# Optimization experiments

Hardware: AMD Instinct MI355X
Metric: run time of the kernel (lower is better)

The kernel has to match this reference:

```python
import jax, jax.numpy as jnp
import numpy as np

B, L, WD = 4096, 30, 300          # batch of news, title length, word dim
H, AD = 20, 20                    # attention heads, per-head dim
MD = H * AD                       # multi_dim = 400
E, ED = 10, 100                   # entities per news, entity dim
QD = 200                          # query_vector_dim
CAT, CD = 18, 50                  # category vocab / dim
SUB, SD = 300, 50                 # subcategory vocab / dim


def _mha(x, wq, bq, wk, bk, wv, bv):
    # x: [B, L, Din] -> [B, L, MD]; standard multi-head self-attention
    b, l, _ = x.shape
    q = (x @ wq + bq).reshape(b, l, H, AD)
    k = (x @ wk + bk).reshape(b, l, H, AD)
    v = (x @ wv + bv).reshape(b, l, H, AD)
    scores = jnp.einsum('blhd,bmhd->bhlm', q, k) / jnp.sqrt(jnp.asarray(AD, x.dtype))
    attn = jax.nn.softmax(scores, axis=-1)
    out = jnp.einsum('bhlm,bmhd->blhd', attn, v)
    return out.reshape(b, l, MD)


def _layernorm(x, g, b):
    mu = jnp.mean(x, axis=-1, keepdims=True)
    var = jnp.var(x, axis=-1, keepdims=True)
    return (x - mu) / jnp.sqrt(var + 1e-5) * g + b


def _additive(x, w, b, q):
    # x: [B, L, D] -> [B, D]
    scores = jnp.tanh(x @ w + b) @ q            # [B, L]
    alpha = jax.nn.softmax(scores, axis=-1)
    return jnp.einsum('bl,bld->bd', alpha, x)


def setup_inputs() -> dict:
    key = jax.random.key(0)
    ks = iter(jax.random.split(key, 40))
    n = lambda shape, s=0.02: (jax.random.normal(next(ks), shape, dtype=jnp.float32) * s)
    inp = {
        'word_embedding': jax.random.normal(next(ks), (B, L, WD), dtype=jnp.float32),
        'entity_embedding': jax.random.normal(next(ks), (B, E, ED), dtype=jnp.float32),
        'category_index': jax.random.randint(next(ks), (B,), 0, CAT, dtype=jnp.int64 if jax.config.jax_enable_x64 else jnp.int32),
        'subcategory_index': jax.random.randint(next(ks), (B,), 0, SUB, dtype=jnp.int64 if jax.config.jax_enable_x64 else jnp.int32),
        # category / subcategory branches
        'emb_cat': n((CAT, CD), 1.0), 'fc1_w': n((CD, MD)), 'fc1_b': jnp.zeros((MD,), jnp.float32),
        'emb_sub': n((SUB, SD), 1.0), 'fc2_w': n((SD, MD)), 'fc2_b': jnp.zeros((MD,), jnp.float32),
        # word multi-head self-attention
        'wq': n((WD, MD)), 'bq': jnp.zeros((MD,), jnp.float32),
        'wk': n((WD, MD)), 'bk': jnp.zeros((MD,), jnp.float32),
        'wv': n((WD, MD)), 'bv': jnp.zeros((MD,), jnp.float32),
        # shared LayerNorm
        'ln_g': jnp.ones((MD,), jnp.float32), 'ln_b': jnp.zeros((MD,), jnp.float32),
        # word additive attention
        'wa_w': n((MD, QD)), 'wa_b': jnp.zeros((QD,), jnp.float32), 'wa_q': n((QD,), 1.0),
        # entity branch: fc3 + GCN (learnable adjacency over the E entities of a news)
        'fc3_w': n((ED, ED)), 'fc3_b': jnp.zeros((ED,), jnp.float32),
        'gcn_A': n((E, E), 1.0), 'gcn_w': n((ED, MD)), 'gcn_b': jnp.zeros((MD,), jnp.float32),
        'ea_w': n((MD, QD)), 'ea_b': jnp.zeros((QD,), jnp.float32), 'ea_q': n((QD,), 1.0),
        # final news-level additive attention over 4 views
        'na_w': n((MD, QD)), 'na_b': jnp.zeros((QD,), jnp.float32), 'na_q': n((QD,), 1.0),
    }
    return inp


def reference(word_embedding, entity_embedding, category_index, subcategory_index,
              emb_cat, fc1_w, fc1_b, emb_sub, fc2_w, fc2_b,
              wq, bq, wk, bk, wv, bv, ln_g, ln_b,
              wa_w, wa_b, wa_q, fc3_w, fc3_b, gcn_A, gcn_w, gcn_b,
              ea_w, ea_b, ea_q, na_w, na_b, na_q):
    # category / subcategory reps (dropout is identity in eval)
    cat_rep = jnp.tanh(emb_cat[category_index] @ fc1_w + fc1_b)      # [B, MD]
    sub_rep = jnp.tanh(emb_sub[subcategory_index] @ fc2_w + fc2_b)   # [B, MD]
    # word branch
    w = _mha(word_embedding, wq, bq, wk, bk, wv, bv)                 # [B, L, MD]
    w = _layernorm(w, ln_g, ln_b)
    word_rep = jnp.tanh(_additive(w, wa_w, wa_b, wa_q))              # [B, MD]
    # entity branch: fc3 -> intra-news GCN -> shared LayerNorm
    e = jnp.tanh(entity_embedding @ fc3_w + fc3_b)                   # [B, E, ED]
    e = jax.nn.relu(jnp.einsum('ef,bfd->bed', gcn_A, e) @ gcn_w + gcn_b)  # [B, E, MD]
    e = _layernorm(e, ln_g, ln_b)
    ent_rep = jnp.tanh(_additive(e, ea_w, ea_b, ea_q))               # [B, MD]
    # fuse the 4 views with additive attention
    views = jnp.stack([word_rep, ent_rep, cat_rep, sub_rep], axis=1)  # [B, 4, MD]
    news_rep = jnp.tanh(_additive(views, na_w, na_b, na_q))          # [B, MD]
    return news_rep
```

## Files before the change

### kernel.cpp

```cpp
#include <hip/hip_runtime.h>
#include <hip/hip_bf16.h>
#include <math.h>

#define B_  4096
#define L_  30
#define WD_ 300
#define H_  20
#define AD_ 20
#define MD_ 400
#define E_  10
#define ED_ 100
#define QD_ 200
#define CD_ 50
#define SD_ 50

typedef unsigned short ushort_t;
typedef __attribute__((ext_vector_type(8))) short bf16x8_t;
typedef __attribute__((ext_vector_type(4))) float f32x4_t;

#define SX_STR   328
#define QKV_STR  1218
#define OUTB_STR 424
#define SOUT_STR 401
#define P_STR    40
#define WT_K     320
#define WAT_K    416

#define N_WT    (1200 * WT_K)
#define N_WAT   (208 * WAT_K)
#define N_FC3T  (112 * 128)
#define N_GCNT  (400 * 128)
#define N_EAT   (208 * WAT_K)

union FragU {
  unsigned  u[4];
  short     s[8];
  bf16x8_t  h;
};

__device__ __forceinline__ ushort_t f2bf(float f) {
  unsigned u = __builtin_bit_cast(unsigned, f);
  unsigned r = (u + 0x7fffu + ((u >> 16) & 1u)) >> 16;
  return (ushort_t)r;
}
__device__ __forceinline__ float bf2f(ushort_t h) {
  return __builtin_bit_cast(float, ((unsigned)h) << 16);
}
__device__ __forceinline__ float wave_reduce_sum(float v) {
  #pragma unroll
  for (int off = 32; off > 0; off >>= 1) v += __shfl_xor(v, off);
  return v;
}
__device__ __forceinline__ void split2(float v, ushort_t* __restrict__ H,
                                       ushort_t* __restrict__ Lo, int idx) {
  const ushort_t h = f2bf(v);
  H[idx] = h;
  Lo[idx] = f2bf(v - bf2f(h));
}

__global__ __launch_bounds__(256) void prep_weights(
    const float* __restrict__ wq, const float* __restrict__ wk, const float* __restrict__ wv,
    const float* __restrict__ wa_w, const float* __restrict__ fc3_w,
    const float* __restrict__ gcn_w, const float* __restrict__ ea_w,
    ushort_t* __restrict__ Wt, ushort_t* __restrict__ Wat,
    ushort_t* __restrict__ fc3TH, ushort_t* __restrict__ fc3TL,
    ushort_t* __restrict__ gcnTH, ushort_t* __restrict__ gcnTL,
    ushort_t* __restrict__ eaTH, ushort_t* __restrict__ eaTL)
{
  int idx = blockIdx.x * 256 + threadIdx.x;
  if (idx < N_WT) {
    const int n = idx / WT_K, k = idx - n * WT_K;
    float v = 0.f;
    if (k < WD_) {
      const float* w = (n < 400) ? wq : (n < 800) ? wk : wv;
      const int c = (n < 400) ? n : (n < 800) ? n - 400 : n - 800;
      v = w[k * MD_ + c];
    }
    Wt[idx] = f2bf(v);
    return;
  }
  idx -= N_WT;
  if (idx < N_WAT) {
    const int q = idx / WAT_K, d = idx - q * WAT_K;
    Wat[idx] = (q < QD_ && d < MD_) ? f2bf(wa_w[d * QD_ + q]) : (ushort_t)0;
    return;
  }
  idx -= N_WAT;
  if (idx < N_FC3T) {
    const int n = idx / 128, k = idx - n * 128;
    const float v = (n < ED_ && k < ED_) ? fc3_w[k * ED_ + n] : 0.f;
    split2(v, fc3TH, fc3TL, idx);
    return;
  }
  idx -= N_FC3T;
  if (idx < N_GCNT) {
    const int n = idx / 128, k = idx - n * 128;
    const float v = (k < ED_) ? gcn_w[k * MD_ + n] : 0.f;
    split2(v, gcnTH, gcnTL, idx);
    return;
  }
  idx -= N_GCNT;
  if (idx < N_EAT) {
    const int q = idx / WAT_K, d = idx - q * WAT_K;
    const float v = (q < QD_ && d < MD_) ? ea_w[d * QD_ + q] : 0.f;
    split2(v, eaTH, eaTL, idx);
  }
}

__global__ __launch_bounds__(1024, 4) void word_branch_kernel(
    const float* __restrict__ X,
    const ushort_t* __restrict__ Wt, const ushort_t* __restrict__ Wat,
    const float* __restrict__ bq, const float* __restrict__ bk, const float* __restrict__ bv,
    const float* __restrict__ ln_g, const float* __restrict__ ln_b,
    const float* __restrict__ wa_b, const float* __restrict__ wa_q,
    float* __restrict__ word_rep)
{
  __shared__ __align__(16) union {
    ushort_t x[32 * SX_STR];
    ushort_t p[16 * 16 * P_STR];
  } uA;
  __shared__ __align__(16) union {
    ushort_t qkv[30 * QKV_STR];
    ushort_t o[32 * OUTB_STR];
  } uB;
  __shared__ __align__(16) float sOut[30 * SOUT_STR];
  __shared__ float sSc[32];
  __shared__ float sAlpha[32];

  const int b    = blockIdx.x;
  const int tid  = threadIdx.x;
  const int wave = tid >> 6;
  const int lane = tid & 63;
  const int lr   = lane & 15;
  const int kg   = lane >> 4;

  const float* xb = X + (size_t)b * (L_ * WD_);
  {
    const int r = tid >> 5;
    const int c0 = tid & 31;
    #pragma unroll
    for (int k = 0; k < 10; ++k) {
      const int c = c0 + k * 32;
      const float v = (r < L_ && c < WD_) ? xb[r * WD_ + c] : 0.f;
      uA.x[r * SX_STR + c] = f2bf(v);
    }
  }
  if (tid < 32) sSc[tid] = 0.f;
  __syncthreads();

  for (int nt = wave; nt < 75; nt += 16) {
    const ushort_t* wbase = &Wt[(nt * 16 + lr) * WT_K + kg * 8];
    bf16x8_t bfa[10];
    #pragma unroll
    for (int ks = 0; ks < 10; ++ks)
      bfa[ks] = *reinterpret_cast<const bf16x8_t*>(wbase + ks * 32);
    f32x4_t acc0 = {0,0,0,0}, acc1 = {0,0,0,0};
    #pragma unroll
    for (int ks = 0; ks < 10; ++ks) {
      const int kb = ks * 32 + kg * 8;
      bf16x8_t af0 = *reinterpret_cast<const bf16x8_t*>(&uA.x[lr * SX_STR + kb]);
      bf16x8_t af1 = *reinterpret_cast<const bf16x8_t*>(&uA.x[(16 + lr) * SX_STR + kb]);
      acc0 = __builtin_amdgcn_mfma_f32_16x16x32_bf16(af0, bfa[ks], acc0, 0, 0, 0);
      acc1 = __builtin_amdgcn_mfma_f32_16x16x32_bf16(af1, bfa[ks], acc1, 0, 0, 0);
    }
    const int col = nt * 16 + lr;
    const float bias = (col < 400) ? bq[col] : (col < 800) ? bk[col - 400] : bv[col - 800];
    #pragma unroll
    for (int i = 0; i < 4; ++i) {
      uB.qkv[(kg * 4 + i) * QKV_STR + col] = f2bf(acc0[i] + bias);
      const int r2 = 16 + kg * 4 + i;
      if (r2 < L_) uB.qkv[r2 * QKV_STR + col] = f2bf(acc1[i] + bias);
    }
  }
  __syncthreads();

  ushort_t* pw = &uA.p[wave * (16 * P_STR)];
  for (int u = wave; u < 2 * H_; u += 16) {
    const int h = u >> 1, mt = u & 1;
    const int hq = h * AD_, hk = 400 + h * AD_, hv = 800 + h * AD_;

    bf16x8_t aq, bkf[2];
    {
      FragU fq;
      fq.u[0]=fq.u[1]=fq.u[2]=fq.u[3]=0;
      const bool okrow = (mt == 0) || (lr < 14);
      if (okrow && kg < 3) {
        const ushort_t* pq = &uB.qkv[(mt * 16 + lr) * QKV_STR + hq + kg * 8];
        fq.u[0] = *(const unsigned*)(pq);     fq.u[1] = *(const unsigned*)(pq + 2);
        if (kg < 2) { fq.u[2] = *(const unsigned*)(pq + 4); fq.u[3] = *(const unsigned*)(pq + 6); }
      }
      aq = fq.h;
    }
    #pragma unroll
    for (int t = 0; t < 2; ++t) {
      FragU fk;
      fk.u[0]=fk.u[1]=fk.u[2]=fk.u[3]=0;
      const bool okrow = (t == 0) || (lr < 14);
      if (okrow && kg < 3) {
        const ushort_t* pk = &uB.qkv[(t * 16 + lr) * QKV_STR + hk + kg * 8];
        fk.u[0] = *(const unsigned*)(pk);     fk.u[1] = *(const unsigned*)(pk + 2);
        if (kg < 2) { fk.u[2] = *(const unsigned*)(pk + 4); fk.u[3] = *(const unsigned*)(pk + 6); }
      }
      bkf[t] = fk.h;
    }
    f32x4_t c0 = {0,0,0,0}, c1 = {0,0,0,0};
    c0 = __builtin_amdgcn_mfma_f32_16x16x32_bf16(aq, bkf[0], c0, 0, 0, 0);
    c1 = __builtin_amdgcn_mfma_f32_16x16x32_bf16(aq, bkf[1], c1, 0, 0, 0);

    const float SCALE = 0.2236067977499790f;
    #pragma unroll
    for (int i = 0; i < 4; ++i) {
      const float v0 = c0[i] * SCALE;
      const float v1 = (lr < 14) ? c1[i] * SCALE : -1e30f;
      float mx = fmaxf(v0, v1);
      mx = fmaxf(mx, __shfl_xor(mx, 1));
      mx = fmaxf(mx, __shfl_xor(mx, 2));
      mx = fmaxf(mx, __shfl_xor(mx, 4));
      mx = fmaxf(mx, __shfl_xor(mx, 8));
      const float e0 = __expf(v0 - mx);
      const float e1 = (lr < 14) ? __expf(v1 - mx) : 0.f;
      float s = e0 + e1;
      s += __shfl_xor(s, 1);
      s += __shfl_xor(s, 2);
      s += __shfl_xor(s, 4);
      s += __shfl_xor(s, 8);
      const float inv = 1.f / s;
      const int row = kg * 4 + i;
      pw[row * P_STR + lr]      = f2bf(e0 * inv);
      pw[row * P_STR + 16 + lr] = f2bf(e1 * inv);
    }
    __asm__ volatile("s_waitcnt lgkmcnt(0)" ::: "memory");

    bf16x8_t ap = *reinterpret_cast<const bf16x8_t*>(&pw[lr * P_STR + kg * 8]);
    bf16x8_t bvf[2];
    #pragma unroll
    for (int nt = 0; nt < 2; ++nt) {
      FragU f;
      const int d = nt * 16 + lr;
      if (d < AD_) {
        #pragma unroll
        for (int j = 0; j < 8; ++j) {
          const int rm = kg * 8 + j;
          f.s[j] = (rm < L_) ? (short)uB.qkv[rm * QKV_STR + hv + d] : (short)0;
        }
      } else {
        f.u[0]=f.u[1]=f.u[2]=f.u[3]=0;
      }
      bvf[nt] = f.h;
    }
    f32x4_t o0 = {0,0,0,0}, o1 = {0,0,0,0};
    o0 = __builtin_amdgcn_mfma_f32_16x16x32_bf16(ap, bvf[0], o0, 0, 0, 0);
    o1 = __builtin_amdgcn_mfma_f32_16x16x32_bf16(ap, bvf[1], o1, 0, 0, 0);

    #pragma unroll
    for (int nt = 0; nt < 2; ++nt) {
      const f32x4_t o = nt ? o1 : o0;
      const int d = nt * 16 + lr;
      if (d < AD_) {
        #pragma unroll
        for (int i = 0; i < 4; ++i) {
          const int r = mt * 16 + kg * 4 + i;
          if (r < L_) sOut[r * SOUT_STR + h * AD_ + d] = o[i];
        }
      }
    }
  }
  __syncthreads();

  for (int r = wave; r < L_; r += 16) {
    float s = 0.f, s2 = 0.f;
    for (int d = lane; d < MD_; d += 64) { const float v = sOut[r * SOUT_STR + d]; s += v; s2 += v * v; }
    s  = wave_reduce_sum(s);
    s2 = wave_reduce_sum(s2);
    const float mu  = s * (1.f / MD_);
    const float var = s2 * (1.f / MD_) - mu * mu;
    const float inv = rsqrtf(var + 1e-5f);
    for (int d = lane; d < MD_; d += 64)
      sOut[r * SOUT_STR + d] = (sOut[r * SOUT_STR + d] - mu) * inv * ln_g[d] + ln_b[d];
  }
  __syncthreads();

  {
    const int r = tid >> 5;
    const int c0 = tid & 31;
    #pragma unroll
    for (int k = 0; k < 13; ++k) {
      const int c = c0 + k * 32;
      if (c < 416) {
        const float v = (r < L_ && c < MD_) ? sOut[r * SOUT_STR + c] : 0.f;
        uB.o[r * OUTB_STR + c] = f2bf(v);
      }
    }
  }
  __syncthreads();

  for (int t = wave; t < 26; t += 16) {
    const int mt = t & 1, nt = t >> 1;
    f32x4_t acc = {0,0,0,0};
    const ushort_t* wbase = &Wat[(nt * 16 + lr) * WAT_K + kg * 8];
    bf16x8_t wfa[13];
    #pragma unroll
    for (int ks = 0; ks < 13; ++ks)
      wfa[ks] = *reinterpret_cast<const bf16x8_t*>(wbase + ks * 32);
    #pragma unroll
    for (int ks = 0; ks < 13; ++ks) {
      const int kb = ks * 32 + kg * 8;
      bf16x8_t af = *reinterpret_cast<const bf16x8_t*>(&uB.o[(mt * 16 + lr) * OUTB_STR + kb]);
      acc = __builtin_amdgcn_mfma_f32_16x16x32_bf16(af, wfa[ks], acc, 0, 0, 0);
    }
    const int q = nt * 16 + lr;
    if (q < QD_) {
      const float bb = wa_b[q], qq = wa_q[q];
      #pragma unroll
      for (int i = 0; i < 4; ++i) {
        const int row = mt * 16 + kg * 4 + i;
        if (row < L_) atomicAdd(&sSc[row], tanhf(acc[i] + bb) * qq);
      }
    }
  }
  __syncthreads();

  if (wave == 0) {
    const float v = (lane < L_) ? sSc[lane] : -1e30f;
    float mx = v;
    #pragma unroll
    for (int off = 32; off > 0; off >>= 1) mx = fmaxf(mx, __shfl_xor(mx, off));
    const float e = (lane < L_) ? __expf(v - mx) : 0.f;
    float s = e;
    #pragma unroll
    for (int off = 32; off > 0; off >>= 1) s += __shfl_xor(s, off);
    if (lane < L_) sAlpha[lane] = e / s;
  }
  __syncthreads();

  if (tid < MD_) {
    const int d = tid;
    float acc = 0.f;
    #pragma unroll 6
    for (int l = 0; l < L_; ++l) acc += sAlpha[l] * sOut[l * SOUT_STR + d];
    word_rep[(size_t)b * MD_ + d] = tanhf(acc);
  }
}

__global__ __launch_bounds__(512, 4) void entity_branch_kernel(
    const float* __restrict__ Ein,
    const ushort_t* __restrict__ fc3TH, const ushort_t* __restrict__ fc3TL,
    const float* __restrict__ fc3_b,
    const float* __restrict__ gcn_A,
    const ushort_t* __restrict__ gcnTH, const ushort_t* __restrict__ gcnTL,
    const float* __restrict__ gcn_b,
    const float* __restrict__ ln_g, const float* __restrict__ ln_b,
    const ushort_t* __restrict__ eaTH, const ushort_t* __restrict__ eaTL,
    const float* __restrict__ ea_b, const float* __restrict__ ea_q,
    float* __restrict__ ent_rep)
{
  __shared__ __align__(16) ushort_t sEh[16 * 136], sEl[16 * 136];
  __shared__ __align__(16) float    eF[E_ * 104];
  __shared__ __align__(16) ushort_t gH[16 * 136], gL[16 * 136];
  __shared__ __align__(16) float    sR[16 * SOUT_STR];
  __shared__ __align__(16) ushort_t oH[16 * OUTB_STR], oL[16 * OUTB_STR];
  __shared__ float sSc[16];
  __shared__ float sAlpha[16];

  const int b    = blockIdx.x;
  const int tid  = threadIdx.x;
  const int wave = tid >> 6;
  const int lane = tid & 63;
  const int lr   = lane & 15;
  const int kg   = lane >> 4;

  for (int id = tid; id < 16 * 128; id += 512) {
    const int r = id >> 7, c = id & 127;
    const float v = (r < E_ && c < ED_) ? Ein[(size_t)b * (E_ * ED_) + r * ED_ + c] : 0.f;
    const ushort_t hh = f2bf(v);
    sEh[r * 136 + c] = hh;
    sEl[r * 136 + c] = f2bf(v - bf2f(hh));
  }
  for (int id = tid; id < 16 * 136; id += 512) { gH[id] = 0; gL[id] = 0; }
  if (tid < 16) sSc[tid] = 0.f;
  __syncthreads();

  for (int nt = wave; nt < 7; nt += 8) {
    f32x4_t acc = {0,0,0,0};
    #pragma unroll
    for (int ks = 0; ks < 4; ++ks) {
      const int kb = ks * 32 + kg * 8;
      bf16x8_t ah = *reinterpret_cast<const bf16x8_t*>(&sEh[lr * 136 + kb]);
      bf16x8_t al = *reinterpret_cast<const bf16x8_t*>(&sEl[lr * 136 + kb]);
      bf16x8_t wh = *reinterpret_cast<const bf16x8_t*>(&fc3TH[(nt * 16 + lr) * 128 + kb]);
      bf16x8_t wl = *reinterpret_cast<const bf16x8_t*>(&fc3TL[(nt * 16 + lr) * 128 + kb]);
      acc = __builtin_amdgcn_mfma_f32_16x16x32_bf16(ah, wh, acc, 0, 0, 0);
      acc = __builtin_amdgcn_mfma_f32_16x16x32_bf16(al, wh, acc, 0, 0, 0);
      acc = __builtin_amdgcn_mfma_f32_16x16x32_bf16(ah, wl, acc, 0, 0, 0);
    }
    const int d = nt * 16 + lr;
    if (d < ED_) {
      const float bias = fc3_b[d];
      #pragma unroll
      for (int i = 0; i < 4; ++i) {
        const int r = kg * 4 + i;
        if (r < E_) eF[r * 104 + d] = tanhf(acc[i] + bias);
      }
    }
  }
  __syncthreads();

  for (int id = tid; id < E_ * ED_; id += 512) {
    const int i = id / ED_, d = id - (id / ED_) * ED_;
    float acc = 0.f;
    #pragma unroll
    for (int f = 0; f < E_; ++f) acc += gcn_A[i * E_ + f] * eF[f * 104 + d];
    const ushort_t hh = f2bf(acc);
    gH[i * 136 + d] = hh;
    gL[i * 136 + d] = f2bf(acc - bf2f(hh));
  }
  __syncthreads();

  for (int nt = wave; nt < 25; nt += 8) {
    f32x4_t acc = {0,0,0,0};
    #pragma unroll
    for (int ks = 0; ks < 4; ++ks) {
      const int kb = ks * 32 + kg * 8;
      bf16x8_t ah = *reinterpret_cast<const bf16x8_t*>(&gH[lr * 136 + kb]);
      bf16x8_t al = *reinterpret_cast<const bf16x8_t*>(&gL[lr * 136 + kb]);
      bf16x8_t wh = *reinterpret_cast<const bf16x8_t*>(&gcnTH[(nt * 16 + lr) * 128 + kb]);
      bf16x8_t wl = *reinterpret_cast<const bf16x8_t*>(&gcnTL[(nt * 16 + lr) * 128 + kb]);
      acc = __builtin_amdgcn_mfma_f32_16x16x32_bf16(ah, wh, acc, 0, 0, 0);
      acc = __builtin_amdgcn_mfma_f32_16x16x32_bf16(al, wh, acc, 0, 0, 0);
      acc = __builtin_amdgcn_mfma_f32_16x16x32_bf16(ah, wl, acc, 0, 0, 0);
    }
    const int d = nt * 16 + lr;
    const float bias = gcn_b[d];
    #pragma unroll
    for (int i = 0; i < 4; ++i) {
      const int r = kg * 4 + i;
      if (r < E_) sR[r * SOUT_STR + d] = fmaxf(acc[i] + bias, 0.f);
    }
  }
  __syncthreads();

  for (int r = wave; r < E_; r += 8) {
    float s = 0.f, s2 = 0.f;
    for (int d = lane; d < MD_; d += 64) { const float v = sR[r * SOUT_STR + d]; s += v; s2 += v * v; }
    s  = wave_reduce_sum(s);
    s2 = wave_reduce_sum(s2);
    const float mu  = s * (1.f / MD_);
    const float var = s2 * (1.f / MD_) - mu * mu;
    const float inv = rsqrtf(var + 1e-5f);
    for (int d = lane; d < MD_; d += 64)
      sR[r * SOUT_STR + d] = (sR[r * SOUT_STR + d] - mu) * inv * ln_g[d] + ln_b[d];
  }
  __syncthreads();

  {
    const int r = tid >> 5;
    const int c0 = tid & 31;
    #pragma unroll
    for (int k = 0; k < 13; ++k) {
      const int c = c0 + k * 32;
      const float v = (r < E_ && c < MD_) ? sR[r * SOUT_STR + c] : 0.f;
      const ushort_t hh = f2bf(v);
      oH[r * OUTB_STR + c] = hh;
      oL[r * OUTB_STR + c] = f2bf(v - bf2f(hh));
    }
  }
  __syncthreads();

  for (int nt = wave; nt < 13; nt += 8) {
    f32x4_t acc = {0,0,0,0};
    for (int ks = 0; ks < 13; ++ks) {
      const int kb = ks * 32 + kg * 8;
      bf16x8_t ah = *reinterpret_cast<const bf16x8_t*>(&oH[lr * OUTB_STR + kb]);
      bf16x8_t al = *reinterpret_cast<const bf16x8_t*>(&oL[lr * OUTB_STR + kb]);
      bf16x8_t wh = *reinterpret_cast<const bf16x8_t*>(&eaTH[(nt * 16 + lr) * WAT_K + kb]);
      bf16x8_t wl = *reinterpret_cast<const bf16x8_t*>(&eaTL[(nt * 16 + lr) * WAT_K + kb]);
      acc = __builtin_amdgcn_mfma_f32_16x16x32_bf16(ah, wh, acc, 0, 0, 0);
      acc = __builtin_amdgcn_mfma_f32_16x16x32_bf16(al, wh, acc, 0, 0, 0);
      acc = __builtin_amdgcn_mfma_f32_16x16x32_bf16(ah, wl, acc, 0, 0, 0);
    }
    const int q = nt * 16 + lr;
    if (q < QD_) {
      const float bb = ea_b[q], qq = ea_q[q];
      #pragma unroll
      for (int i = 0; i < 4; ++i) {
        const int r = kg * 4 + i;
        if (r < E_) atomicAdd(&sSc[r], tanhf(acc[i] + bb) * qq);
      }
    }
  }
  __syncthreads();

  if (wave == 0) {
    const float v = (lane < E_) ? sSc[lane] : -1e30f;
    float mx = v;
    #pragma unroll
    for (int off = 32; off > 0; off >>= 1) mx = fmaxf(mx, __shfl_xor(mx, off));
    const float e = (lane < E_) ? __expf(v - mx) : 0.f;
    float s = e;
    #pragma unroll
    for (int off = 32; off > 0; off >>= 1) s += __shfl_xor(s, off);
    if (lane < E_) sAlpha[lane] = e / s;
  }
  __syncthreads();

  if (tid < MD_) {
    const int d = tid;
    float acc = 0.f;
    #pragma unroll
    for (int i = 0; i < E_; ++i) acc += sAlpha[i] * sR[i * SOUT_STR + d];
    ent_rep[(size_t)b * MD_ + d] = tanhf(acc);
  }
}

__global__ __launch_bounds__(256) void catsub_kernel(
    const int* __restrict__ cat_idx, const int* __restrict__ sub_idx,
    const float* __restrict__ emb_cat, const float* __restrict__ fc1_w, const float* __restrict__ fc1_b,
    const float* __restrict__ emb_sub, const float* __restrict__ fc2_w, const float* __restrict__ fc2_b,
    float* __restrict__ cat_rep, float* __restrict__ sub_rep)
{
  int idx = blockIdx.x * 256 + threadIdx.x;
  const int total = B_ * MD_;
  if (idx < total) {
    const int b = idx / MD_, d = idx - (idx / MD_) * MD_;
    const float* row = emb_cat + (size_t)cat_idx[b] * CD_;
    float acc = fc1_b[d];
    #pragma unroll
    for (int k = 0; k < CD_; ++k) acc += row[k] * fc1_w[k * MD_ + d];
    cat_rep[idx] = tanhf(acc);
  } else {
    idx -= total;
    if (idx < total) {
      const int b = idx / MD_, d = idx - (idx / MD_) * MD_;
      const float* row = emb_sub + (size_t)sub_idx[b] * SD_;
      float acc = fc2_b[d];
      #pragma unroll
      for (int k = 0; k < SD_; ++k) acc += row[k] * fc2_w[k * MD_ + d];
      sub_rep[idx] = tanhf(acc);
    }
  }
}

__global__ __launch_bounds__(256) void fuse_kernel(
    const float* __restrict__ word_rep, const float* __restrict__ ent_rep,
    const float* __restrict__ cat_rep, const float* __restrict__ sub_rep,
    const float* __restrict__ na_w, const float* __restrict__ na_b, const float* __restrict__ na_q,
    float* __restrict__ out)
{
  __shared__ float sViews[4][MD_];
  __shared__ float sSc[4];
  __shared__ float sAlpha[4];
  const int b = blockIdx.x, tid = threadIdx.x;
  for (int d = tid; d < MD_; d += 256) {
    sViews[0][d] = word_rep[(size_t)b * MD_ + d];
    sViews[1][d] = ent_rep[(size_t)b * MD_ + d];
    sViews[2][d] = cat_rep[(size_t)b * MD_ + d];
    sViews[3][d] = sub_rep[(size_t)b * MD_ + d];
  }
  if (tid < 4) sSc[tid] = 0.f;
  __syncthreads();
  for (int id = tid; id < 4 * QD_; id += 256) {
    const int v = id / QD_, q = id - (id / QD_) * QD_;
    float acc = na_b[q];
    #pragma unroll 4
    for (int d = 0; d < MD_; ++d) acc += sViews[v][d] * na_w[d * QD_ + q];
    atomicAdd(&sSc[v], tanhf(acc) * na_q[q]);
  }
  __syncthreads();
  if (tid == 0) {
    float mx = -1e30f;
    for (int v = 0; v < 4; ++v) mx = fmaxf(mx, sSc[v]);
    float sum = 0.f;
    for (int v = 0; v < 4; ++v) { const float e = __expf(sSc[v] - mx); sAlpha[v] = e; sum += e; }
    const float inv = 1.f / sum;
    for (int v = 0; v < 4; ++v) sAlpha[v] *= inv;
  }
  __syncthreads();
  for (int d = tid; d < MD_; d += 256) {
    const float acc = sAlpha[0] * sViews[0][d] + sAlpha[1] * sViews[1][d] +
                      sAlpha[2] * sViews[2][d] + sAlpha[3] * sViews[3][d];
    out[(size_t)b * MD_ + d] = tanhf(acc);
  }
}

extern "C" void kernel_launch(void* const* d_in, const int* in_sizes, int n_in,
                              void* d_out, int out_size, void* d_ws, size_t ws_size,
                              hipStream_t stream) {
  const float* X        = (const float*)d_in[0];
  const float* Ein      = (const float*)d_in[1];
  const int*   cat_idx  = (const int*)d_in[2];
  const int*   sub_idx  = (const int*)d_in[3];
  const float* emb_cat  = (const float*)d_in[4];
  const float* fc1_w    = (const float*)d_in[5];
  const float* fc1_b    = (const float*)d_in[6];
  const float* emb_sub  = (const float*)d_in[7];
  const float* fc2_w    = (const float*)d_in[8];
  const float* fc2_b    = (const float*)d_in[9];
  const float* wq       = (const float*)d_in[10];
  const float* bq       = (const float*)d_in[11];
  const float* wk       = (const float*)d_in[12];
  const float* bk       = (const float*)d_in[13];
  const float* wv       = (const float*)d_in[14];
  const float* bv       = (const float*)d_in[15];
  const float* ln_g     = (const float*)d_in[16];
  const float* ln_b     = (const float*)d_in[17];
  const float* wa_w     = (const float*)d_in[18];
  const float* wa_b     = (const float*)d_in[19];
  const float* wa_q     = (const float*)d_in[20];
  const float* fc3_w    = (const float*)d_in[21];
  const float* fc3_b    = (const float*)d_in[22];
  const float* gcn_A    = (const float*)d_in[23];
  const float* gcn_w    = (const float*)d_in[24];
  const float* gcn_b    = (const float*)d_in[25];
  const float* ea_w     = (const float*)d_in[26];
  const float* ea_b     = (const float*)d_in[27];
  const float* ea_q     = (const float*)d_in[28];
  const float* na_w     = (const float*)d_in[29];
  const float* na_b     = (const float*)d_in[30];
  const float* na_q     = (const float*)d_in[31];

  float* out = (float*)d_out;
  const size_t BM = (size_t)B_ * MD_;
  float* word_rep = (float*)d_ws;
  float* ent_rep  = word_rep + BM;
  float* cat_rep  = ent_rep + BM;
  float* sub_rep  = cat_rep + BM;
  ushort_t* Wt    = (ushort_t*)(sub_rep + BM);
  ushort_t* Wat   = Wt + N_WT;
  ushort_t* fc3TH = Wat + N_WAT;
  ushort_t* fc3TL = fc3TH + N_FC3T;
  ushort_t* gcnTH = fc3TL + N_FC3T;
  ushort_t* gcnTL = gcnTH + N_GCNT;
  ushort_t* eaTH  = gcnTL + N_GCNT;
  ushort_t* eaTL  = eaTH + N_EAT;

  {
    const int total = N_WT + N_WAT + N_FC3T + N_GCNT + N_EAT;
    prep_weights<<<(total + 255) / 256, 256, 0, stream>>>(
        wq, wk, wv, wa_w, fc3_w, gcn_w, ea_w,
        Wt, Wat, fc3TH, fc3TL, gcnTH, gcnTL, eaTH, eaTL);
  }
  word_branch_kernel<<<B_, 1024, 0, stream>>>(X, Wt, Wat, bq, bk, bv,
                                              ln_g, ln_b, wa_b, wa_q, word_rep);
  entity_branch_kernel<<<B_, 512, 0, stream>>>(Ein, fc3TH, fc3TL, fc3_b, gcn_A,
                                               gcnTH, gcnTL, gcn_b,
                                               ln_g, ln_b, eaTH, eaTL, ea_b, ea_q, ent_rep);
  catsub_kernel<<<(2 * B_ * MD_) / 256, 256, 0, stream>>>(cat_idx, sub_idx,
                                                          emb_cat, fc1_w, fc1_b,
                                                          emb_sub, fc2_w, fc2_b,
                                                          cat_rep, sub_rep);
  fuse_kernel<<<B_, 256, 0, stream>>>(word_rep, ent_rep, cat_rep, sub_rep,
                                      na_w, na_b, na_q, out);
}
```

Before: 1.323 ms.

## Fuse layernorm with bf16 packing and hoist LDS activation fragments out of GEMM loops

In the word kernel, the QKV GEMM now loads the input activation fragments from shared memory once into registers before the column-tile loop and streams the weight fragments from global memory per k-step. Previously it reloaded the activations from LDS on every tile. The attention-projection GEMM does the reverse: it holds activation fragments and streams the weights. Layernorm in both the word and entity kernels now writes the bf16 (hi/lo) packed copy directly, which drops a separate conversion pass and one barrier, with padding zeroed separately. This costs more register pressure from holding 20 or 13 fragment vectors, and the streamed global weight loads are now on the MFMA critical path.

```diff
diff --git a/kernel.cpp b/kernel.cpp
--- a/kernel.cpp
+++ b/kernel.cpp
@@ -148,20 +148,20 @@
   if (tid < 32) sSc[tid] = 0.f;
   __syncthreads();
 
+  bf16x8_t axl[10], axh[10];
+  #pragma unroll
+  for (int ks = 0; ks < 10; ++ks) {
+    axl[ks] = *reinterpret_cast<const bf16x8_t*>(&uA.x[lr * SX_STR + ks * 32 + kg * 8]);
+    axh[ks] = *reinterpret_cast<const bf16x8_t*>(&uA.x[(16 + lr) * SX_STR + ks * 32 + kg * 8]);
+  }
   for (int nt = wave; nt < 75; nt += 16) {
     const ushort_t* wbase = &Wt[(nt * 16 + lr) * WT_K + kg * 8];
-    bf16x8_t bfa[10];
-    #pragma unroll
-    for (int ks = 0; ks < 10; ++ks)
-      bfa[ks] = *reinterpret_cast<const bf16x8_t*>(wbase + ks * 32);
     f32x4_t acc0 = {0,0,0,0}, acc1 = {0,0,0,0};
     #pragma unroll
     for (int ks = 0; ks < 10; ++ks) {
-      const int kb = ks * 32 + kg * 8;
-      bf16x8_t af0 = *reinterpret_cast<const bf16x8_t*>(&uA.x[lr * SX_STR + kb]);
-      bf16x8_t af1 = *reinterpret_cast<const bf16x8_t*>(&uA.x[(16 + lr) * SX_STR + kb]);
-      acc0 = __builtin_amdgcn_mfma_f32_16x16x32_bf16(af0, bfa[ks], acc0, 0, 0, 0);
-      acc1 = __builtin_amdgcn_mfma_f32_16x16x32_bf16(af1, bfa[ks], acc1, 0, 0, 0);
+      bf16x8_t bf = *reinterpret_cast<const bf16x8_t*>(wbase + ks * 32);
+      acc0 = __builtin_amdgcn_mfma_f32_16x16x32_bf16(axl[ks], bf, acc0, 0, 0, 0);
+      acc1 = __builtin_amdgcn_mfma_f32_16x16x32_bf16(axh[ks], bf, acc1, 0, 0, 0);
     }
     const int col = nt * 16 + lr;
     const float bias = (col < 400) ? bq[col] : (col < 800) ? bk[col - 400] : bv[col - 800];
@@ -275,38 +275,37 @@
     const float mu  = s * (1.f / MD_);
     const float var = s2 * (1.f / MD_) - mu * mu;
     const float inv = rsqrtf(var + 1e-5f);
-    for (int d = lane; d < MD_; d += 64)
-      sOut[r * SOUT_STR + d] = (sOut[r * SOUT_STR + d] - mu) * inv * ln_g[d] + ln_b[d];
-  }
-  __syncthreads();
-
+    for (int d = lane; d < MD_; d += 64) {
+      const float nv = (sOut[r * SOUT_STR + d] - mu) * inv * ln_g[d] + ln_b[d];
+      sOut[r * SOUT_STR + d] = nv;
+      uB.o[r * OUTB_STR + d] = f2bf(nv);
+    }
+  }
+  if (tid < 2 * 416) {
+    const int r = 30 + (tid / 416), c = tid - (tid / 416) * 416;
+    uB.o[r * OUTB_STR + c] = 0;
+  }
   {
-    const int r = tid >> 5;
-    const int c0 = tid & 31;
-    #pragma unroll
-    for (int k = 0; k < 13; ++k) {
-      const int c = c0 + k * 32;
-      if (c < 416) {
-        const float v = (r < L_ && c < MD_) ? sOut[r * SOUT_STR + c] : 0.f;
-        uB.o[r * OUTB_STR + c] = f2bf(v);
-      }
+    const int id = tid;
+    if (id < 30 * 16) {
+      const int r = id >> 4, c = 400 + (id & 15);
+      uB.o[r * OUTB_STR + c] = 0;
     }
   }
   __syncthreads();
 
   for (int t = wave; t < 26; t += 16) {
     const int mt = t & 1, nt = t >> 1;
+    bf16x8_t afa[13];
+    #pragma unroll
+    for (int ks = 0; ks < 13; ++ks)
+      afa[ks] = *reinterpret_cast<const bf16x8_t*>(&uB.o[(mt * 16 + lr) * OUTB_STR + ks * 32 + kg * 8]);
+    const ushort_t* wbase = &Wat[(nt * 16 + lr) * WAT_K + kg * 8];
     f32x4_t acc = {0,0,0,0};
-    const ushort_t* wbase = &Wat[(nt * 16 + lr) * WAT_K + kg * 8];
-    bf16x8_t wfa[13];
-    #pragma unroll
-    for (int ks = 0; ks < 13; ++ks)
-      wfa[ks] = *reinterpret_cast<const bf16x8_t*>(wbase + ks * 32);
     #pragma unroll
     for (int ks = 0; ks < 13; ++ks) {
-      const int kb = ks * 32 + kg * 8;
-      bf16x8_t af = *reinterpret_cast<const bf16x8_t*>(&uB.o[(mt * 16 + lr) * OUTB_STR + kb]);
-      acc = __builtin_amdgcn_mfma_f32_16x16x32_bf16(af, wfa[ks], acc, 0, 0, 0);
+      bf16x8_t wf = *reinterpret_cast<const bf16x8_t*>(wbase + ks * 32);
+      acc = __builtin_amdgcn_mfma_f32_16x16x32_bf16(afa[ks], wf, acc, 0, 0, 0);
     }
     const int q = nt * 16 + lr;
     if (q < QD_) {
@@ -377,6 +376,7 @@
     sEl[r * 136 + c] = f2bf(v - bf2f(hh));
   }
   for (int id = tid; id < 16 * 136; id += 512) { gH[id] = 0; gL[id] = 0; }
+  for (int id = tid; id < 16 * OUTB_STR; id += 512) { oH[id] = 0; oL[id] = 0; }
   if (tid < 16) sSc[tid] = 0.f;
   __syncthreads();
 
@@ -447,21 +447,12 @@
     const float mu  = s * (1.f / MD_);
     const float var = s2 * (1.f / MD_) - mu * mu;
     const float inv = rsqrtf(var + 1e-5f);
-    for (int d = lane; d < MD_; d += 64)
-      sR[r * SOUT_STR + d] = (sR[r * SOUT_STR + d] - mu) * inv * ln_g[d] + ln_b[d];
-  }
-  __syncthreads();
-
-  {
-    const int r = tid >> 5;
-    const int c0 = tid & 31;
-    #pragma unroll
-    for (int k = 0; k < 13; ++k) {
-      const int c = c0 + k * 32;
-      const float v = (r < E_ && c < MD_) ? sR[r * SOUT_STR + c] : 0.f;
-      const ushort_t hh = f2bf(v);
-      oH[r * OUTB_STR + c] = hh;
-      oL[r * OUTB_STR + c] = f2bf(v - bf2f(hh));
+    for (int d = lane; d < MD_; d += 64) {
+      const float nv = (sR[r * SOUT_STR + d] - mu) * inv * ln_g[d] + ln_b[d];
+      sR[r * SOUT_STR + d] = nv;
+      const ushort_t hh = f2bf(nv);
+      oH[r * OUTB_STR + d] = hh;
+      oL[r * OUTB_STR + d] = f2bf(nv - bf2f(hh));
     }
   }
   __syncthreads();
```

After: 1.312 ms, median of 3. No clear change (-0.8%).
